# Kernel tuning notes

Hardware: AMD Instinct MI355X
Metric: run time of the kernel (lower is better)

Reference implementation:

```python
import jax, jax.numpy as jnp
import numpy as np

H = 256          # h_dim
SEQ_LEN = 10     # max history length
B = 2048         # number of queries with non-empty history
N = 327680       # total flattened neighbors across all (query, timestep) segments
NUM_SEG = B * SEQ_LEN
NUM_ENT = 20000
NUM_REL = 200


def setup_inputs() -> dict:
    key = jax.random.key(0)
    ks = jax.random.split(key, 9)
    s = jax.random.randint(ks[0], (B,), 0, NUM_ENT)
    r = jax.random.randint(ks[1], (B,), 0, NUM_REL)
    nbr_ids = jax.random.randint(ks[2], (N,), 0, NUM_ENT)
    seg_ids = jnp.sort(jax.random.randint(ks[3], (N,), 0, NUM_SEG))
    ent_embeds = jax.random.normal(ks[4], (NUM_ENT, H), dtype=jnp.float32)
    rel_embeds = jax.random.normal(ks[5], (NUM_REL, H), dtype=jnp.float32)
    W_attn = jax.random.normal(ks[6], (3 * H, H), dtype=jnp.float32) * 0.05
    b_attn = jax.random.normal(ks[7], (H,), dtype=jnp.float32) * 0.05
    v_s = jax.random.normal(ks[8], (H, 1), dtype=jnp.float32) * 0.05
    return {"s": s, "r": r, "nbr_ids": nbr_ids, "seg_ids": seg_ids,
            "ent_embeds": ent_embeds, "rel_embeds": rel_embeds,
            "W_attn": W_attn, "b_attn": b_attn, "v_s": v_s}


def reference(s, r, nbr_ids, seg_ids, ent_embeds, rel_embeds, W_attn, b_attn, v_s):
    # Per-neighbor gathers. Each neighbor belongs to segment seg = q*SEQ_LEN + t.
    q = seg_ids // SEQ_LEN                              # query index per neighbor [N]
    em = ent_embeds[nbr_ids]                            # [N, H] neighbor embeddings
    s_emb = ent_embeds[s]                               # [B, H]
    r_emb = rel_embeds[r]                               # [B, H]
    ss = s_emb[q]                                       # [N, H]
    rr = r_emb[q]                                       # [N, H]
    # Score: tanh(Linear(3H -> H)) @ v_s  -> scalar per neighbor
    x = jnp.concatenate([em, ss, rr], axis=1)           # [N, 3H]
    scores = (jnp.tanh(x @ W_attn + b_attn) @ v_s)[:, 0]  # [N]
    # Segment softmax over neighbors within each (query, timestep) segment.
    m = jax.ops.segment_max(scores, seg_ids, num_segments=NUM_SEG)  # [S]
    e = jnp.exp(scores - m[seg_ids])                    # [N]
    denom = jax.ops.segment_sum(e, seg_ids, num_segments=NUM_SEG)   # [S]
    w = e / denom[seg_ids]                              # [N]
    # Weighted sum of neighbor embeddings per segment (scatter-reduce).
    agg = jax.ops.segment_sum(w[:, None] * em, seg_ids, num_segments=NUM_SEG)  # [S, H]
    counts = jax.ops.segment_sum(jnp.ones_like(scores), seg_ids, num_segments=NUM_SEG)
    mask = (counts > 0).astype(em.dtype).reshape(B, SEQ_LEN, 1)     # present timesteps
    agg = agg.reshape(B, SEQ_LEN, H)
    ss_t = jnp.broadcast_to(s_emb[:, None, :], (B, SEQ_LEN, H))
    rr_t = jnp.broadcast_to(r_emb[:, None, :], (B, SEQ_LEN, H))
    # Padded [B, SEQ_LEN, 3H] sequence tensor (rows for empty segments are zero,
    # matching the torch code's zero-initialized padded tensor). Dropout p=0.0.
    out = jnp.concatenate([agg, ss_t, rr_t], axis=2) * mask
    return out
```

## Files before the change

### kernel.cpp

```cpp
#include <hip/hip_runtime.h>
#include <hip/hip_bf16.h>

#define H 256
#define SEQ 10
#define C2LOG2E 2.8853900817779268f
#define LOG2E 1.4426950408889634f

typedef __attribute__((ext_vector_type(8))) short bf16x8;
typedef __attribute__((ext_vector_type(4))) float f32x4;

__device__ __forceinline__ unsigned short f2bf(float x) {
    union { float f; unsigned u; } v; v.f = x;
    unsigned r = v.u + 0x7fff + ((v.u >> 16) & 1);
    return (unsigned short)(r >> 16);
}
__device__ __forceinline__ float bf2f(unsigned short b) {
    union { unsigned u; float f; } v; v.u = ((unsigned)b) << 16;
    return v.f;
}
__device__ __forceinline__ float fexp2(float x) {
    return __builtin_amdgcn_exp2f(x);
}

__global__ void prep_kernel(const float* __restrict__ W,
                            unsigned short* __restrict__ Wt,
                            const int* __restrict__ seg_ids,
                            int* __restrict__ seg_start,
                            int nWt, int n, int num_seg) {
    if ((int)blockIdx.x < nWt) {
        int idx = blockIdx.x * 256 + threadIdx.x;
        if (idx >= H * 3 * H) return;
        int nn = idx / (3 * H), k = idx % (3 * H);
        Wt[idx] = f2bf(C2LOG2E * W[k * H + nn]);
    } else {
        int j = (blockIdx.x - nWt) * 256 + threadIdx.x;
        if (j >= n) return;
        int cur = seg_ids[j];
        int prev = (j == 0) ? -1 : seg_ids[j - 1];
        for (int s2 = prev + 1; s2 <= cur; s2++) seg_start[s2] = j;
        if (j == n - 1)
            for (int s2 = cur + 1; s2 <= num_seg; s2++) seg_start[s2] = n;
    }
}

__global__ void gemm_bf16_kernel(const float* __restrict__ entf,
                                 const int* __restrict__ sidx,
                                 const int* __restrict__ ridx,
                                 const float* __restrict__ rel,
                                 const unsigned short* __restrict__ Wt,
                                 const float* __restrict__ bias,
                                 unsigned short* __restrict__ comb,
                                 unsigned short* __restrict__ qpart,
                                 int nEntBlk, int M0, int M1) {
    __shared__ unsigned short As[64][40];
    __shared__ unsigned short Bs[256][40];
    bool isEnt = (int)blockIdx.x < nEntBlk;
    int m0 = (isEnt ? blockIdx.x : (blockIdx.x - nEntBlk)) * 64;
    int M = isEnt ? M0 : M1;
    int K = isEnt ? H : 2 * H;
    int k0 = isEnt ? 0 : H;
    int ldo = isEnt ? 512 : H;
    unsigned short* outp = isEnt ? comb : qpart;

    int t = threadIdx.x;
    int sr = t >> 2;
    int sc = (t & 3) * 8;
    int wave = t >> 6, lane = t & 63;
    int lr = lane & 15, lg = lane >> 4;

    f32x4 acc[4][4];
#pragma unroll
    for (int i = 0; i < 4; i++)
#pragma unroll
        for (int jn = 0; jn < 4; jn++) acc[i][jn] = (f32x4){0.f, 0.f, 0.f, 0.f};

    for (int kk = 0; kk < K; kk += 32) {
        bf16x8 av = {};
        int gm = m0 + sr;
        if (gm < M) {
            const float* src;
            if (isEnt) {
                src = entf + (size_t)gm * H + kk + sc;
            } else {
                int k = kk + sc;
                src = (k < H) ? (entf + (size_t)sidx[gm] * H + k)
                              : (rel + (size_t)ridx[gm] * H + (k - H));
            }
            float4 f0 = *reinterpret_cast<const float4*>(src);
            float4 f1 = *reinterpret_cast<const float4*>(src + 4);
            av[0] = (short)f2bf(f0.x); av[1] = (short)f2bf(f0.y);
            av[2] = (short)f2bf(f0.z); av[3] = (short)f2bf(f0.w);
            av[4] = (short)f2bf(f1.x); av[5] = (short)f2bf(f1.y);
            av[6] = (short)f2bf(f1.z); av[7] = (short)f2bf(f1.w);
            if (isEnt)
                *reinterpret_cast<bf16x8*>(comb + (size_t)gm * 512 + 256 + kk + sc) = av;
        }
        *reinterpret_cast<bf16x8*>(&As[sr][sc]) = av;
#pragma unroll
        for (int r4 = 0; r4 < 4; r4++) {
            int row = r4 * 64 + sr;
            bf16x8 bv = *reinterpret_cast<const bf16x8*>(
                Wt + (size_t)row * (3 * H) + k0 + kk + sc);
            *reinterpret_cast<bf16x8*>(&Bs[row][sc]) = bv;
        }
        __syncthreads();

        bf16x8 afr[4], bfr[4];
#pragma unroll
        for (int am = 0; am < 4; am++)
            afr[am] = *reinterpret_cast<const bf16x8*>(&As[am * 16 + lr][lg * 8]);
#pragma unroll
        for (int bn = 0; bn < 4; bn++)
            bfr[bn] = *reinterpret_cast<const bf16x8*>(&Bs[wave * 64 + bn * 16 + lr][lg * 8]);
#pragma unroll
        for (int am = 0; am < 4; am++)
#pragma unroll
            for (int bn = 0; bn < 4; bn++)
                acc[am][bn] = __builtin_amdgcn_mfma_f32_16x16x32_bf16(
                    afr[am], bfr[bn], acc[am][bn], 0, 0, 0);
        __syncthreads();
    }

#pragma unroll
    for (int bn = 0; bn < 4; bn++) {
        int col = wave * 64 + bn * 16 + lr;
        float bv = isEnt ? 0.f : C2LOG2E * bias[col];
#pragma unroll
        for (int am = 0; am < 4; am++) {
#pragma unroll
            for (int rr = 0; rr < 4; rr++) {
                int row = m0 + am * 16 + lg * 4 + rr;
                if (row < M)
                    outp[(size_t)row * ldo + col] = f2bf(acc[am][bn][rr] + bv);
            }
        }
    }
}

__global__ void __launch_bounds__(256, 4)
fused_agg_kernel(const int* __restrict__ nbr_ids,
                 const int* __restrict__ seg_start,
                 const unsigned short* __restrict__ comb,
                 const unsigned short* __restrict__ qpartbf,
                 const float* __restrict__ v_s,
                 const float* __restrict__ ent_embeds,
                 const float* __restrict__ rel_embeds,
                 const int* __restrict__ s,
                 const int* __restrict__ r,
                 float* __restrict__ out, int num_seg) {
    int wid = blockIdx.x * 4 + (threadIdx.x >> 6);
    int nw = gridDim.x * 4;
    int lane = threadIdx.x & 63;
    int g = lane >> 4, li = lane & 15;
    int cb = li * 16;
    int c4 = lane * 4;

    float vm2[16];
    float vsum = 0.f;
    {
        const float4* vp = reinterpret_cast<const float4*>(v_s + cb);
#pragma unroll
        for (int k = 0; k < 4; k++) {
            float4 tv = vp[k];
            vm2[4 * k + 0] = -2.f * tv.x; vm2[4 * k + 1] = -2.f * tv.y;
            vm2[4 * k + 2] = -2.f * tv.z; vm2[4 * k + 3] = -2.f * tv.w;
            vsum += tv.x + tv.y + tv.z + tv.w;
        }
    }

    for (int seg = wid; seg < num_seg; seg += nw) {
        int start = seg_start[seg], end = seg_start[seg + 1];
        int b = seg / SEQ;
        float* orow = out + (size_t)seg * (3 * H);

        if (start == end) {
            float4 z = {0.f, 0.f, 0.f, 0.f};
            *reinterpret_cast<float4*>(orow + c4) = z;
            *reinterpret_cast<float4*>(orow + H + c4) = z;
            *reinterpret_cast<float4*>(orow + 2 * H + c4) = z;
            continue;
        }

        float qv[16];
        {
            bf16x8 qa = *reinterpret_cast<const bf16x8*>(qpartbf + (size_t)b * H + cb);
            bf16x8 qb = *reinterpret_cast<const bf16x8*>(qpartbf + (size_t)b * H + cb + 8);
#pragma unroll
            for (int k = 0; k < 8; k++) {
                qv[k] = bf2f((unsigned short)qa[k]);
                qv[8 + k] = bf2f((unsigned short)qb[k]);
            }
        }

        float acc[16];
#pragma unroll
        for (int k = 0; k < 16; k++) acc[k] = 0.f;
        float lpart = 0.f;

        int cc = end - start;
        int nitm = (cc + 3) >> 2;

        int j0 = min(g, cc - 1);
        const unsigned short* row = comb + (size_t)nbr_ids[start + j0] * 512 + cb;
        bf16x8 p0 = *reinterpret_cast<const bf16x8*>(row);
        bf16x8 p1 = *reinterpret_cast<const bf16x8*>(row + 8);

        for (int ji = 0; ji < nitm; ji++) {
            bf16x8 e0 = *reinterpret_cast<const bf16x8*>(row + 256);
            bf16x8 e1 = *reinterpret_cast<const bf16x8*>(row + 264);
            int jn = min(4 * (ji + 1) + g, cc - 1);
            const unsigned short* rown = comb + (size_t)nbr_ids[start + jn] * 512 + cb;
            bf16x8 p0n = *reinterpret_cast<const bf16x8*>(rown);
            bf16x8 p1n = *reinterpret_cast<const bf16x8*>(rown + 8);

            float s16 = 0.f;
#pragma unroll
            for (int k = 0; k < 8; k++) {
                float r0 = __builtin_amdgcn_rcpf(
                    fexp2(bf2f((unsigned short)p0[k]) + qv[k]) + 1.f);
                s16 = fmaf(vm2[k], r0, s16);
                float r1 = __builtin_amdgcn_rcpf(
                    fexp2(bf2f((unsigned short)p1[k]) + qv[8 + k]) + 1.f);
                s16 = fmaf(vm2[8 + k], r1, s16);
            }
            s16 += vsum;
            s16 += __shfl_xor(s16, 1);
            s16 += __shfl_xor(s16, 2);
            s16 += __shfl_xor(s16, 4);
            s16 += __shfl_xor(s16, 8);
            float e = fexp2(s16 * LOG2E);
            e = (4 * ji + g < cc) ? e : 0.f;
            lpart += e;
#pragma unroll
            for (int k = 0; k < 8; k++) {
                acc[k] = fmaf(e, bf2f((unsigned short)e0[k]), acc[k]);
                acc[8 + k] = fmaf(e, bf2f((unsigned short)e1[k]), acc[8 + k]);
            }
            p0 = p0n; p1 = p1n; row = rown;
        }

        lpart += __shfl_xor(lpart, 16);
        lpart += __shfl_xor(lpart, 32);
#pragma unroll
        for (int k = 0; k < 16; k++) {
            acc[k] += __shfl_xor(acc[k], 16);
            acc[k] += __shfl_xor(acc[k], 32);
        }
        float invl = 1.f / lpart;

        float4 o;
#pragma unroll
        for (int k = 0; k < 4; k++) {
            float v0 = acc[k], v1 = acc[4 + k], v2 = acc[8 + k], v3 = acc[12 + k];
            float pick = (g == 0) ? v0 : (g == 1) ? v1 : (g == 2) ? v2 : v3;
            if (k == 0) o.x = pick * invl;
            else if (k == 1) o.y = pick * invl;
            else if (k == 2) o.z = pick * invl;
            else o.w = pick * invl;
        }
        *reinterpret_cast<float4*>(orow + cb + 4 * g) = o;
        *reinterpret_cast<float4*>(orow + H + c4) =
            *reinterpret_cast<const float4*>(ent_embeds + (size_t)s[b] * H + c4);
        *reinterpret_cast<float4*>(orow + 2 * H + c4) =
            *reinterpret_cast<const float4*>(rel_embeds + (size_t)r[b] * H + c4);
    }
}

extern "C" void kernel_launch(void* const* d_in, const int* in_sizes, int n_in,
                              void* d_out, int out_size, void* d_ws, size_t ws_size,
                              hipStream_t stream) {
    const int* s = (const int*)d_in[0];
    const int* r = (const int*)d_in[1];
    const int* nbr_ids = (const int*)d_in[2];
    const int* seg_ids = (const int*)d_in[3];
    const float* ent_embeds = (const float*)d_in[4];
    const float* rel_embeds = (const float*)d_in[5];
    const float* W_attn = (const float*)d_in[6];
    const float* b_attn = (const float*)d_in[7];
    const float* v_s = (const float*)d_in[8];
    float* out = (float*)d_out;

    int B = in_sizes[0];
    int N = in_sizes[2];
    int num_ent = in_sizes[4] / H;
    int num_seg = B * SEQ;

    char* ws = (char*)d_ws;
    unsigned short* comb = (unsigned short*)ws;
    unsigned short* Wt = comb + (size_t)num_ent * 512;
    unsigned short* qpartbf = Wt + (size_t)H * 3 * H;
    int* seg_start = (int*)(qpartbf + (size_t)B * H);

    int nWt = (H * 3 * H + 255) / 256;
    int nSeg = (N + 255) / 256;
    prep_kernel<<<nWt + nSeg, 256, 0, stream>>>(W_attn, Wt, seg_ids, seg_start,
                                                nWt, N, num_seg);

    int nEntBlk = (num_ent + 63) / 64;
    int nQBlk = B / 64;
    gemm_bf16_kernel<<<nEntBlk + nQBlk, 256, 0, stream>>>(
        ent_embeds, s, r, rel_embeds, Wt, b_attn, comb, qpartbf,
        nEntBlk, num_ent, B);

    fused_agg_kernel<<<2048, 256, 0, stream>>>(
        nbr_ids, seg_start, comb, qpartbf, v_s,
        ent_embeds, rel_embeds, s, r, out, num_seg);
}
```

Baseline: 93.44 us.

## Load GEMM B fragments from global directly and prefetch neighbor embeddings

The GEMM kernel drops the shared-memory staging of the weight tile and has each lane load its MFMA B fragments straight from global memory. This removes LDS writes, LDS reads and part of the barrier cost, but adds redundant global loads per wave. The aggregation loop now prefetches the next neighbor's embedding half (e0/e1) one iteration ahead along with the projection half, which hides gather latency. The score dot product is also split into two independent FMA chains to shorten the dependency chain.

```diff
diff --git a/kernel.cpp b/kernel.cpp
--- a/kernel.cpp
+++ b/kernel.cpp
@@ -53,7 +53,6 @@
                                  unsigned short* __restrict__ qpart,
                                  int nEntBlk, int M0, int M1) {
     __shared__ unsigned short As[64][40];
-    __shared__ unsigned short Bs[256][40];
     bool isEnt = (int)blockIdx.x < nEntBlk;
     int m0 = (isEnt ? blockIdx.x : (blockIdx.x - nEntBlk)) * 64;
     int M = isEnt ? M0 : M1;
@@ -73,6 +72,11 @@
     for (int i = 0; i < 4; i++)
 #pragma unroll
         for (int jn = 0; jn < 4; jn++) acc[i][jn] = (f32x4){0.f, 0.f, 0.f, 0.f};
+
+    const unsigned short* bp[4];
+#pragma unroll
+    for (int bn = 0; bn < 4; bn++)
+        bp[bn] = Wt + (size_t)(wave * 64 + bn * 16 + lr) * (3 * H) + k0 + lg * 8;
 
     for (int kk = 0; kk < K; kk += 32) {
         bf16x8 av = {};
@@ -96,22 +100,17 @@
                 *reinterpret_cast<bf16x8*>(comb + (size_t)gm * 512 + 256 + kk + sc) = av;
         }
         *reinterpret_cast<bf16x8*>(&As[sr][sc]) = av;
-#pragma unroll
-        for (int r4 = 0; r4 < 4; r4++) {
-            int row = r4 * 64 + sr;
-            bf16x8 bv = *reinterpret_cast<const bf16x8*>(
-                Wt + (size_t)row * (3 * H) + k0 + kk + sc);
-            *reinterpret_cast<bf16x8*>(&Bs[row][sc]) = bv;
-        }
+
+        bf16x8 bfr[4];
+#pragma unroll
+        for (int bn = 0; bn < 4; bn++)
+            bfr[bn] = *reinterpret_cast<const bf16x8*>(bp[bn] + kk);
+
         __syncthreads();
-
-        bf16x8 afr[4], bfr[4];
+        bf16x8 afr[4];
 #pragma unroll
         for (int am = 0; am < 4; am++)
             afr[am] = *reinterpret_cast<const bf16x8*>(&As[am * 16 + lr][lg * 8]);
-#pragma unroll
-        for (int bn = 0; bn < 4; bn++)
-            bfr[bn] = *reinterpret_cast<const bf16x8*>(&Bs[wave * 64 + bn * 16 + lr][lg * 8]);
 #pragma unroll
         for (int am = 0; am < 4; am++)
 #pragma unroll
@@ -204,26 +203,26 @@
         const unsigned short* row = comb + (size_t)nbr_ids[start + j0] * 512 + cb;
         bf16x8 p0 = *reinterpret_cast<const bf16x8*>(row);
         bf16x8 p1 = *reinterpret_cast<const bf16x8*>(row + 8);
+        bf16x8 e0 = *reinterpret_cast<const bf16x8*>(row + 256);
+        bf16x8 e1 = *reinterpret_cast<const bf16x8*>(row + 264);
 
         for (int ji = 0; ji < nitm; ji++) {
-            bf16x8 e0 = *reinterpret_cast<const bf16x8*>(row + 256);
-            bf16x8 e1 = *reinterpret_cast<const bf16x8*>(row + 264);
             int jn = min(4 * (ji + 1) + g, cc - 1);
             const unsigned short* rown = comb + (size_t)nbr_ids[start + jn] * 512 + cb;
             bf16x8 p0n = *reinterpret_cast<const bf16x8*>(rown);
             bf16x8 p1n = *reinterpret_cast<const bf16x8*>(rown + 8);
-
-            float s16 = 0.f;
+            bf16x8 e0n = *reinterpret_cast<const bf16x8*>(rown + 256);
+            bf16x8 e1n = *reinterpret_cast<const bf16x8*>(rown + 264);
+
+            float sa = 0.f, sb = 0.f;
 #pragma unroll
             for (int k = 0; k < 8; k++) {
-                float r0 = __builtin_amdgcn_rcpf(
-                    fexp2(bf2f((unsigned short)p0[k]) + qv[k]) + 1.f);
-                s16 = fmaf(vm2[k], r0, s16);
-                float r1 = __builtin_amdgcn_rcpf(
-                    fexp2(bf2f((unsigned short)p1[k]) + qv[8 + k]) + 1.f);
-                s16 = fmaf(vm2[8 + k], r1, s16);
-            }
-            s16 += vsum;
+                sa = fmaf(vm2[k], __builtin_amdgcn_rcpf(
+                        fexp2(bf2f((unsigned short)p0[k]) + qv[k]) + 1.f), sa);
+                sb = fmaf(vm2[8 + k], __builtin_amdgcn_rcpf(
+                        fexp2(bf2f((unsigned short)p1[k]) + qv[8 + k]) + 1.f), sb);
+            }
+            float s16 = sa + sb + vsum;
             s16 += __shfl_xor(s16, 1);
             s16 += __shfl_xor(s16, 2);
             s16 += __shfl_xor(s16, 4);
@@ -236,7 +235,7 @@
                 acc[k] = fmaf(e, bf2f((unsigned short)e0[k]), acc[k]);
                 acc[8 + k] = fmaf(e, bf2f((unsigned short)e1[k]), acc[8 + k]);
             }
-            p0 = p0n; p1 = p1n; row = rown;
+            p0 = p0n; p1 = p1n; e0 = e0n; e1 = e1n;
         }
 
         lpart += __shfl_xor(lpart, 16);
```

New measurement: 93.70 us. About the same (+0.3%).
